# Performance work log

Hardware: AMD Instinct MI355X
Metric: run time of the kernel (lower is better)

Reference implementation:

```python
import jax, jax.numpy as jnp
import numpy as np
from jax import lax

# Config (matches init_kwargs)
E = 8         # num_routed_experts
K = 2         # topk
D = 2048      # d_model
H = 1408      # moe_hidden_dimension
NS = 2        # num_shared_experts
B, T = 2, 2048
EPS = 1e-20   # topk_norm_epsilon
HS = H * NS   # shared expert hidden dim


def setup_inputs() -> dict:
    key = jax.random.key(0)
    ks = jax.random.split(key, 8)
    s = 0.02
    return {
        "x": jax.random.normal(ks[0], (B, T, D), jnp.float32),
        "router_w": jax.random.normal(ks[1], (E, D), jnp.float32) * 0.006,
        # routed experts, stacked: gate/up: [E, D, H], down: [E, H, D]
        "wg": jax.random.normal(ks[2], (E, D, H), jnp.float32) * s,
        "wu": jax.random.normal(ks[3], (E, D, H), jnp.float32) * s,
        "wd": jax.random.normal(ks[4], (E, H, D), jnp.float32) * s,
        # shared expert (single big SwiGLU FFN)
        "sg": jax.random.normal(ks[5], (D, HS), jnp.float32) * s,
        "su": jax.random.normal(ks[6], (D, HS), jnp.float32) * s,
        "sd": jax.random.normal(ks[7], (HS, D), jnp.float32) * s,
    }


def _silu(v):
    return v * jax.nn.sigmoid(v)


def reference(x, router_w, wg, wu, wd, sg, su, sd):
    b, t, d = x.shape
    xf = x.reshape(b * t, d)                       # [N, D]
    n = xf.shape[0]

    # Router: softmax over experts, then top-k masking (DeepSeek style)
    gates = jax.nn.softmax(xf @ router_w.T, axis=-1)           # [N, E]
    topv, topi = lax.top_k(gates, K)                           # [N, K]
    masked = jnp.zeros_like(gates).at[jnp.arange(n)[:, None], topi].set(topv)
    # normalized_moe_gates=True
    masked = masked / (masked.sum(axis=-1, keepdims=True) + EPS)  # [N, E]

    # Per-expert SwiGLU FFN, weighted-accumulated over experts.
    # Mathematically identical to gather/grouped-GEMM/scatter-add combine:
    # tokens with zero gate for expert e contribute 0.
    def step(acc, p):
        wg_e, wu_e, wd_e, g_e = p                  # g_e: [N] gate weights
        y = (_silu(xf @ wg_e) * (xf @ wu_e)) @ wd_e  # [N, D]
        return acc + y * g_e[:, None], None

    routed, _ = lax.scan(step, jnp.zeros_like(xf), (wg, wu, wd, masked.T))

    # Shared experts (dense path applied to every token)
    shared = (_silu(xf @ sg) * (xf @ su)) @ sd      # [N, D]

    return (routed + shared).reshape(b, t, d)
```

## Files before the change

### kernel.cpp

```cpp
#include <hip/hip_runtime.h>
#include <hip/hip_bf16.h>
#include <cstdint>

#define NTOK 4096
#define DMODEL 2048
#define NEXP 8
#define HR 1408
#define HSHARED 2816
#define MAXT64 136
#define MAXT128 72

typedef __attribute__((ext_vector_type(8))) short bf16x8;
typedef __attribute__((ext_vector_type(4))) float f32x4;

__device__ inline unsigned short f2b(float f) {
    unsigned u = __float_as_uint(f);
    u += 0x7fffu + ((u >> 16) & 1u);
    return (unsigned short)(u >> 16);
}
__device__ inline unsigned pack2(float a, float b) {
    return (unsigned)f2b(a) | ((unsigned)f2b(b) << 16);
}

__device__ __forceinline__ void gll16(unsigned short* lds, const unsigned short* g) {
    __builtin_amdgcn_global_load_lds(
        (__attribute__((address_space(1))) void*)g,
        (__attribute__((address_space(3))) void*)lds, 16, 0, 0);
}

__global__ __launch_bounds__(256) void k_router(const float* __restrict__ x,
                                                const float* __restrict__ rw,
                                                int* __restrict__ topi,
                                                float* __restrict__ topw,
                                                int* __restrict__ counts) {
    int gw = (blockIdx.x * 256 + threadIdx.x) >> 6;
    int lane = threadIdx.x & 63;
    if (gw >= NTOK) return;
    const float* xr = x + (size_t)gw * DMODEL;
    float s[NEXP] = {0.f,0.f,0.f,0.f,0.f,0.f,0.f,0.f};
    for (int d = lane; d < DMODEL; d += 64) {
        float xv = xr[d];
#pragma unroll
        for (int e = 0; e < NEXP; e++) s[e] = fmaf(xv, rw[e * DMODEL + d], s[e]);
    }
#pragma unroll
    for (int e = 0; e < NEXP; e++)
        for (int o = 32; o > 0; o >>= 1) s[e] += __shfl_xor(s[e], o, 64);
    if (lane == 0) {
        int i1 = 0;
#pragma unroll
        for (int e = 1; e < NEXP; e++) if (s[e] > s[i1]) i1 = e;
        int i2 = (i1 == 0) ? 1 : 0;
#pragma unroll
        for (int e = 0; e < NEXP; e++) if (e != i1 && s[e] > s[i2]) i2 = e;
        float mx = s[0];
#pragma unroll
        for (int e = 1; e < NEXP; e++) mx = fmaxf(mx, s[e]);
        float den = 0.f, ex[NEXP];
#pragma unroll
        for (int e = 0; e < NEXP; e++) { ex[e] = __expf(s[e] - mx); den += ex[e]; }
        float v1 = ex[i1] / den, v2 = ex[i2] / den;
        float inv = 1.f / (v1 + v2 + 1e-20f);
        topi[2 * gw] = i1; topi[2 * gw + 1] = i2;
        topw[2 * gw] = v1 * inv; topw[2 * gw + 1] = v2 * inv;
        atomicAdd(&counts[i1], 1); atomicAdd(&counts[i2], 1);
    }
}

__global__ void k_scan(int* counts, int* offsets, int* cursors, int* ntiles,
                       int* tile_e, int* tile_r, int step) {
    if (threadIdx.x == 0 && blockIdx.x == 0) {
        int off = 0, nt = 0;
        for (int e = 0; e < NEXP; e++) {
            offsets[e] = off; cursors[e] = off;
            int c = counts[e];
            for (int r = 0; r < c; r += step) { tile_e[nt] = e; tile_r[nt] = r; nt++; }
            off += c;
        }
        ntiles[0] = nt;
    }
}

__global__ __launch_bounds__(256) void k_fill(const int* __restrict__ topi,
                                              const float* __restrict__ topw,
                                              int* cursors, int* at, float* aw) {
    int t = blockIdx.x * 256 + threadIdx.x;
    if (t >= NTOK) return;
#pragma unroll
    for (int k = 0; k < 2; k++) {
        int e = topi[2 * t + k];
        int pos = atomicAdd(&cursors[e], 1);
        at[pos] = t; aw[pos] = topw[2 * t + k];
    }
}

__global__ __launch_bounds__(256) void k_cvt_x(const float* __restrict__ src,
                                               unsigned short* __restrict__ dst) {
    size_t i = ((size_t)blockIdx.x * 256 + threadIdx.x) * 8;
    float4 a = *(const float4*)(src + i);
    float4 b = *(const float4*)(src + i + 4);
    uint4 v; v.x = pack2(a.x, a.y); v.y = pack2(a.z, a.w);
    v.z = pack2(b.x, b.y); v.w = pack2(b.z, b.w);
    *(uint4*)(dst + i) = v;
}

__global__ __launch_bounds__(256) void k_tcvt(const float* __restrict__ src,
                                              unsigned short* __restrict__ dst,
                                              int K, int N) {
    src += (size_t)blockIdx.z * K * N;
    dst += (size_t)blockIdx.z * K * N;
    int n0 = blockIdx.x * 64, k0 = blockIdx.y * 64;
    __shared__ unsigned short T[64][72];
    int t = threadIdx.x;
    int kr = t >> 4, nc = (t & 15) * 4;
#pragma unroll
    for (int i = 0; i < 4; i++) {
        int k = kr + i * 16;
        float4 v = *(const float4*)(src + (size_t)(k0 + k) * N + n0 + nc);
        T[k][nc] = f2b(v.x); T[k][nc + 1] = f2b(v.y);
        T[k][nc + 2] = f2b(v.z); T[k][nc + 3] = f2b(v.w);
    }
    __syncthreads();
    int nr = t >> 3, kc = (t & 7) * 8;
#pragma unroll
    for (int j = 0; j < 2; j++) {
        int n = nr + j * 32;
        unsigned short tmp[8];
#pragma unroll
        for (int u = 0; u < 8; u++) tmp[u] = T[kc + u][n];
        *(uint4*)(dst + (size_t)(n0 + n) * K + k0 + kc) = *(uint4*)tmp;
    }
}


template <bool GATHERED>
__global__ __launch_bounds__(256) void kf_gateup(
    const unsigned short* __restrict__ xb, const unsigned short* __restrict__ BgT,
    const unsigned short* __restrict__ BuT, int K, int Hld, int ebase,
    const int* __restrict__ tile_e, const int* __restrict__ tile_r,
    const int* __restrict__ offsets, const int* __restrict__ counts,
    const int* __restrict__ ntiles, const int* __restrict__ at,
    unsigned short* __restrict__ hout) {
    int m0, mcnt;
    const unsigned short* bgw = BgT;
    const unsigned short* buw = BuT;
    if (GATHERED) {
        if ((int)blockIdx.x >= ntiles[0]) return;
        int e = tile_e[blockIdx.x];
        if (e < ebase || e >= ebase + 4) return;
        int ro = tile_r[blockIdx.x];
        m0 = offsets[e] + ro;
        mcnt = counts[e] - ro; if (mcnt > 128) mcnt = 128;
        size_t wofs = (size_t)(e - ebase) * Hld * K;
        bgw += wofs; buw += wofs;
    } else { m0 = blockIdx.x * 128; mcnt = 128; }
    int n0 = blockIdx.y * 64;

    __shared__ __align__(16) unsigned short As[128 * 64];
    __shared__ __align__(16) unsigned short Bgs[64 * 64];
    __shared__ __align__(16) unsigned short Bus[64 * 64];

    int tid = threadIdx.x;
    int wv = tid >> 6, lane = tid & 63;
    int rbase = tid >> 3;
    int kc = (tid & 7) ^ ((tid >> 3) & 7);
    const unsigned short* arp[4];
#pragma unroll
    for (int j = 0; j < 4; j++) {
        int row = j * 32 + rbase;
        int cl = row < mcnt ? row : mcnt - 1;
        int grow = GATHERED ? at[m0 + cl] : (m0 + cl);
        arp[j] = xb + (size_t)grow * K + kc * 8;
    }
    const unsigned short* bgp[2];
    const unsigned short* bup[2];
#pragma unroll
    for (int j = 0; j < 2; j++) {
        int row = j * 32 + rbase;
        bgp[j] = bgw + (size_t)(n0 + row) * K + kc * 8;
        bup[j] = buw + (size_t)(n0 + row) * K + kc * 8;
    }
    unsigned short* a_l = As + (wv << 6) * 8;
    unsigned short* g_l = Bgs + (wv << 6) * 8;
    unsigned short* u_l = Bus + (wv << 6) * 8;

    int fr = lane & 15, quad = lane >> 4, sw = fr & 7;
    int wm = (wv & 1) << 6, wn = (wv >> 1) << 5;

    f32x4 accg[4][2] = {};
    f32x4 accu[4][2] = {};

    for (int k0 = 0; k0 < K; k0 += 64) {
        __syncthreads();
#pragma unroll
        for (int j = 0; j < 4; j++) gll16(a_l + j * 2048, arp[j] + k0);
#pragma unroll
        for (int j = 0; j < 2; j++) {
            gll16(g_l + j * 2048, bgp[j] + k0);
            gll16(u_l + j * 2048, bup[j] + k0);
        }
        __syncthreads();
#pragma unroll
        for (int s = 0; s < 2; s++) {
            int off = (((s << 2) + quad) ^ sw) << 3;
            bf16x8 a[4], g[2], u[2];
#pragma unroll
            for (int tm = 0; tm < 4; tm++)
                a[tm] = *(const bf16x8*)&As[(wm + tm * 16 + fr) * 64 + off];
#pragma unroll
            for (int tn = 0; tn < 2; tn++) {
                int rb = (wn + tn * 16 + fr) * 64 + off;
                g[tn] = *(const bf16x8*)&Bgs[rb];
                u[tn] = *(const bf16x8*)&Bus[rb];
            }
#pragma unroll
            for (int tm = 0; tm < 4; tm++)
#pragma unroll
                for (int tn = 0; tn < 2; tn++) {
                    accg[tm][tn] = __builtin_amdgcn_mfma_f32_16x16x32_bf16(a[tm], g[tn], accg[tm][tn], 0, 0, 0);
                    accu[tm][tn] = __builtin_amdgcn_mfma_f32_16x16x32_bf16(a[tm], u[tn], accu[tm][tn], 0, 0, 0);
                }
        }
    }
#pragma unroll
    for (int tm = 0; tm < 4; tm++)
#pragma unroll
        for (int r = 0; r < 4; r++) {
            int row = wm + tm * 16 + (quad << 2) + r;
            if (row < mcnt) {
#pragma unroll
                for (int tn = 0; tn < 2; tn++) {
                    float gv = accg[tm][tn][r], uv = accu[tm][tn][r];
                    float hv = (gv / (1.f + __expf(-gv))) * uv;
                    hout[(size_t)(m0 + row) * Hld + n0 + wn + tn * 16 + fr] = f2b(hv);
                }
            }
        }
}

template <bool GATHERED>
__global__ __launch_bounds__(256) void kf_down(
    const unsigned short* __restrict__ h, const unsigned short* __restrict__ BT,
    int K,
    const int* __restrict__ tile_e, const int* __restrict__ tile_r,
    const int* __restrict__ offsets, const int* __restrict__ counts,
    const int* __restrict__ ntiles, const int* __restrict__ at,
    const float* __restrict__ awt, float* __restrict__ out) {
    int m0, mcnt;
    const unsigned short* bw = BT;
    if (GATHERED) {
        if ((int)blockIdx.x >= ntiles[0]) return;
        int e = tile_e[blockIdx.x], ro = tile_r[blockIdx.x];
        m0 = offsets[e] + ro;
        mcnt = counts[e] - ro; if (mcnt > 128) mcnt = 128;
        bw += (size_t)e * DMODEL * K;
    } else { m0 = blockIdx.x * 128; mcnt = 128; }
    int n0 = blockIdx.y * 128;

    __shared__ __align__(16) unsigned short As[128 * 64];
    __shared__ __align__(16) unsigned short Bs[128 * 64];

    int tid = threadIdx.x;
    int wv = tid >> 6, lane = tid & 63;
    int rbase = tid >> 3;
    int kc = (tid & 7) ^ ((tid >> 3) & 7);
    const unsigned short* arp[4];
    const unsigned short* brp[4];
#pragma unroll
    for (int j = 0; j < 4; j++) {
        int row = j * 32 + rbase;
        int cl = row < mcnt ? row : mcnt - 1;
        arp[j] = h + (size_t)(m0 + cl) * K + kc * 8;
        brp[j] = bw + (size_t)(n0 + row) * K + kc * 8;
    }
    unsigned short* a_l = As + (wv << 6) * 8;
    unsigned short* b_l = Bs + (wv << 6) * 8;

    int fr = lane & 15, quad = lane >> 4, sw = fr & 7;
    int wm = (wv & 1) << 6, wn = (wv >> 1) << 6;

    f32x4 acc[4][4] = {};

    for (int k0 = 0; k0 < K; k0 += 64) {
        __syncthreads();
#pragma unroll
        for (int j = 0; j < 4; j++) {
            gll16(a_l + j * 2048, arp[j] + k0);
            gll16(b_l + j * 2048, brp[j] + k0);
        }
        __syncthreads();
#pragma unroll
        for (int s = 0; s < 2; s++) {
            int off = (((s << 2) + quad) ^ sw) << 3;
            bf16x8 a[4], b[4];
#pragma unroll
            for (int tm = 0; tm < 4; tm++)
                a[tm] = *(const bf16x8*)&As[(wm + tm * 16 + fr) * 64 + off];
#pragma unroll
            for (int tn = 0; tn < 4; tn++)
                b[tn] = *(const bf16x8*)&Bs[(wn + tn * 16 + fr) * 64 + off];
#pragma unroll
            for (int tm = 0; tm < 4; tm++)
#pragma unroll
                for (int tn = 0; tn < 4; tn++)
                    acc[tm][tn] = __builtin_amdgcn_mfma_f32_16x16x32_bf16(a[tm], b[tn], acc[tm][tn], 0, 0, 0);
        }
    }
#pragma unroll
    for (int tm = 0; tm < 4; tm++)
#pragma unroll
        for (int r = 0; r < 4; r++) {
            int row = wm + tm * 16 + (quad << 2) + r;
            if (row < mcnt) {
                if (GATHERED) {
                    int tok = at[m0 + row];
                    float w = awt[m0 + row];
#pragma unroll
                    for (int tn = 0; tn < 4; tn++)
                        atomicAdd(&out[(size_t)tok * DMODEL + n0 + wn + tn * 16 + fr],
                                  w * acc[tm][tn][r]);
                } else {
#pragma unroll
                    for (int tn = 0; tn < 4; tn++)
                        out[(size_t)(m0 + row) * DMODEL + n0 + wn + tn * 16 + fr] =
                            acc[tm][tn][r];
                }
            }
        }
}

template <bool GATHERED>
__global__ __launch_bounds__(256) void k_gateup(
    const float* __restrict__ x, const float* __restrict__ Wg,
    const float* __restrict__ Wu, int Hld,
    const int* __restrict__ tile_e, const int* __restrict__ tile_r,
    const int* __restrict__ offsets, const int* __restrict__ counts,
    const int* __restrict__ ntiles, const int* __restrict__ at,
    unsigned short* __restrict__ hout) {
    int m0, mcnt;
    const float* wgp = Wg;
    const float* wup = Wu;
    if (GATHERED) {
        if ((int)blockIdx.x >= ntiles[0]) return;
        int e = tile_e[blockIdx.x], ro = tile_r[blockIdx.x];
        m0 = offsets[e] + ro;
        mcnt = counts[e] - ro; if (mcnt > 64) mcnt = 64;
        size_t wofs = (size_t)e * DMODEL * Hld;
        wgp += wofs; wup += wofs;
    } else { m0 = blockIdx.x * 64; mcnt = 64; }
    int n0 = blockIdx.y * 64;
    __shared__ unsigned short As[64][48];
    __shared__ unsigned short Bgs[64][48];
    __shared__ unsigned short Bus[64][48];
    int tid = threadIdx.x;
    int ai = tid >> 2, ak = (tid & 3) << 3;
    int arowi = m0 + (ai < mcnt ? ai : (mcnt - 1));
    const float* arow = x + (size_t)(GATHERED ? at[arowi] : arowi) * DMODEL;
    int bn = tid >> 2, bk = (tid & 3) << 1;
    const float* bcolg = wgp + (size_t)n0 + bn;
    const float* bcolu = wup + (size_t)n0 + bn;
    int lane = tid & 63, wv = tid >> 6;
    int wm = (wv & 1) << 5, wn = (wv >> 1) << 5;
    int fr = lane & 15, fk = (lane >> 4) << 3;
    f32x4 accg[2][2] = {};
    f32x4 accu[2][2] = {};
    for (int k0 = 0; k0 < DMODEL; k0 += 32) {
        __syncthreads();
        float4 a0 = *(const float4*)(arow + k0 + ak);
        float4 a1 = *(const float4*)(arow + k0 + ak + 4);
        uint4 av; av.x = pack2(a0.x, a0.y); av.y = pack2(a0.z, a0.w);
        av.z = pack2(a1.x, a1.y); av.w = pack2(a1.z, a1.w);
        *(uint4*)&As[ai][ak] = av;
#pragma unroll
        for (int j = 0; j < 4; j++) {
            int kk = bk + (j << 3);
            size_t o0 = (size_t)(k0 + kk) * Hld;
            *(unsigned*)&Bgs[bn][kk] = pack2(bcolg[o0], bcolg[o0 + Hld]);
            *(unsigned*)&Bus[bn][kk] = pack2(bcolu[o0], bcolu[o0 + Hld]);
        }
        __syncthreads();
        bf16x8 af[2], bg[2], bu[2];
#pragma unroll
        for (int t = 0; t < 2; t++) {
            af[t] = *(bf16x8*)&As[wm + t * 16 + fr][fk];
            bg[t] = *(bf16x8*)&Bgs[wn + t * 16 + fr][fk];
            bu[t] = *(bf16x8*)&Bus[wn + t * 16 + fr][fk];
        }
#pragma unroll
        for (int tm = 0; tm < 2; tm++)
#pragma unroll
            for (int tn = 0; tn < 2; tn++) {
                accg[tm][tn] = __builtin_amdgcn_mfma_f32_16x16x32_bf16(af[tm], bg[tn], accg[tm][tn], 0, 0, 0);
                accu[tm][tn] = __builtin_amdgcn_mfma_f32_16x16x32_bf16(af[tm], bu[tn], accu[tm][tn], 0, 0, 0);
            }
    }
    int quad = (lane >> 4) << 2;
#pragma unroll
    for (int tm = 0; tm < 2; tm++)
#pragma unroll
        for (int r = 0; r < 4; r++) {
            int row = wm + tm * 16 + quad + r;
            if (row < mcnt) {
#pragma unroll
                for (int tn = 0; tn < 2; tn++) {
                    float g = accg[tm][tn][r], u = accu[tm][tn][r];
                    float hv = (g / (1.f + __expf(-g))) * u;
                    hout[(size_t)(m0 + row) * Hld + n0 + wn + tn * 16 + fr] = f2b(hv);
                }
            }
        }
}

template <bool GATHERED>
__global__ __launch_bounds__(256) void k_down(
    const unsigned short* __restrict__ h, const float* __restrict__ Wd, int Hld,
    const int* __restrict__ tile_e, const int* __restrict__ tile_r,
    const int* __restrict__ offsets, const int* __restrict__ counts,
    const int* __restrict__ ntiles, const int* __restrict__ at,
    const float* __restrict__ aw, float* __restrict__ out) {
    int m0, mcnt;
    const float* wdp = Wd;
    if (GATHERED) {
        if ((int)blockIdx.x >= ntiles[0]) return;
        int e = tile_e[blockIdx.x], ro = tile_r[blockIdx.x];
        m0 = offsets[e] + ro;
        mcnt = counts[e] - ro; if (mcnt > 64) mcnt = 64;
        wdp += (size_t)e * Hld * DMODEL;
    } else { m0 = blockIdx.x * 64; mcnt = 64; }
    int n0 = blockIdx.y * 64;
    __shared__ unsigned short As[64][48];
    __shared__ unsigned short Bs[64][48];
    int tid = threadIdx.x;
    int ai = tid >> 2, ak = (tid & 3) << 3;
    const unsigned short* arow = h + (size_t)(m0 + (ai < mcnt ? ai : (mcnt - 1))) * Hld;
    int bn = tid >> 2, bk = (tid & 3) << 1;
    const float* bcol = wdp + (size_t)n0 + bn;
    int lane = tid & 63, wv = tid >> 6;
    int wm = (wv & 1) << 5, wn = (wv >> 1) << 5;
    int fr = lane & 15, fk = (lane >> 4) << 3;
    f32x4 acc[2][2] = {};
    for (int k0 = 0; k0 < Hld; k0 += 32) {
        __syncthreads();
        *(uint4*)&As[ai][ak] = *(const uint4*)(arow + k0 + ak);
#pragma unroll
        for (int j = 0; j < 4; j++) {
            int kk = bk + (j << 3);
            size_t o0 = (size_t)(k0 + kk) * DMODEL;
            *(unsigned*)&Bs[bn][kk] = pack2(bcol[o0], bcol[o0 + DMODEL]);
        }
        __syncthreads();
        bf16x8 af[2], bf[2];
#pragma unroll
        for (int t = 0; t < 2; t++) {
            af[t] = *(bf16x8*)&As[wm + t * 16 + fr][fk];
            bf[t] = *(bf16x8*)&Bs[wn + t * 16 + fr][fk];
        }
#pragma unroll
        for (int tm = 0; tm < 2; tm++)
#pragma unroll
            for (int tn = 0; tn < 2; tn++)
                acc[tm][tn] = __builtin_amdgcn_mfma_f32_16x16x32_bf16(af[tm], bf[tn], acc[tm][tn], 0, 0, 0);
    }
    int quad = (lane >> 4) << 2;
#pragma unroll
    for (int tm = 0; tm < 2; tm++)
#pragma unroll
        for (int r = 0; r < 4; r++) {
            int row = wm + tm * 16 + quad + r;
            if (row < mcnt) {
                int mrow = m0 + row;
                int tok = GATHERED ? at[mrow] : mrow;
                float w = GATHERED ? aw[mrow] : 1.f;
#pragma unroll
                for (int tn = 0; tn < 2; tn++)
                    atomicAdd(&out[(size_t)tok * DMODEL + n0 + wn + tn * 16 + fr],
                              w * acc[tm][tn][r]);
            }
        }
}

extern "C" void kernel_launch(void* const* d_in, const int* in_sizes, int n_in,
                              void* d_out, int out_size, void* d_ws, size_t ws_size,
                              hipStream_t stream) {
    (void)in_sizes; (void)n_in;
    const float* x  = (const float*)d_in[0];
    const float* rw = (const float*)d_in[1];
    const float* wg = (const float*)d_in[2];
    const float* wu = (const float*)d_in[3];
    const float* wd = (const float*)d_in[4];
    const float* sg = (const float*)d_in[5];
    const float* su = (const float*)d_in[6];
    const float* sd = (const float*)d_in[7];
    float* out = (float*)d_out;

    int* counts  = (int*)d_ws;
    int* offsets = counts + 8;
    int* cursors = counts + 16;
    int* ntiles  = counts + 24;
    int* tile_e  = counts + 32;
    int* tile_r  = tile_e + 144;
    int* topi    = tile_r + 144;
    float* topw  = (float*)(topi + 8192);
    int* at      = (int*)(topw + 8192);
    float* aw    = (float*)(at + 8192);

    const size_t META = 262144;
    const size_t XB   = (size_t)NTOK * DMODEL * 2;
    const size_t POOL_NEED = 69206016;
    const size_t FAST_NEED = META + XB + POOL_NEED;
    bool fast = ws_size >= FAST_NEED;

    hipMemsetAsync(counts, 0, 32, stream);
    k_router<<<dim3(NTOK / 4), 256, 0, stream>>>(x, rw, topi, topw, counts);
    k_scan<<<1, 64, 0, stream>>>(counts, offsets, cursors, ntiles, tile_e, tile_r,
                                 fast ? 128 : 64);
    k_fill<<<dim3(NTOK / 256), 256, 0, stream>>>(topi, topw, cursors, at, aw);

    if (fast) {
        char* base = (char*)d_ws;
        unsigned short* xb = (unsigned short*)(base + META);
        char* pool = base + META + XB;
        unsigned short* sgT = (unsigned short*)pool;
        unsigned short* suT = (unsigned short*)(pool + 11534336);
        unsigned short* h_s = (unsigned short*)(pool + 23068672);
        unsigned short* sdT = (unsigned short*)(pool + 46137344);
        unsigned short* wgT = (unsigned short*)pool;
        unsigned short* wuT = (unsigned short*)(pool + 23068672);
        unsigned short* h_r = (unsigned short*)(pool + 46137344);
        unsigned short* wdT = (unsigned short*)pool;

        k_cvt_x<<<dim3(4096), 256, 0, stream>>>(x, xb);

        k_tcvt<<<dim3(HSHARED / 64, DMODEL / 64, 1), 256, 0, stream>>>(sg, sgT, DMODEL, HSHARED);
        k_tcvt<<<dim3(HSHARED / 64, DMODEL / 64, 1), 256, 0, stream>>>(su, suT, DMODEL, HSHARED);
        kf_gateup<false><<<dim3(NTOK / 128, HSHARED / 64), 256, 0, stream>>>(
            xb, sgT, suT, DMODEL, HSHARED, 0,
            nullptr, nullptr, nullptr, nullptr, nullptr, nullptr, h_s);
        k_tcvt<<<dim3(DMODEL / 64, HSHARED / 64, 1), 256, 0, stream>>>(sd, sdT, HSHARED, DMODEL);
        kf_down<false><<<dim3(NTOK / 128, DMODEL / 128), 256, 0, stream>>>(
            h_s, sdT, HSHARED,
            nullptr, nullptr, nullptr, nullptr, nullptr, nullptr, nullptr, out);

        k_tcvt<<<dim3(HR / 64, DMODEL / 64, 4), 256, 0, stream>>>(wg, wgT, DMODEL, HR);
        k_tcvt<<<dim3(HR / 64, DMODEL / 64, 4), 256, 0, stream>>>(wu, wuT, DMODEL, HR);
        kf_gateup<true><<<dim3(MAXT128, HR / 64), 256, 0, stream>>>(
            xb, wgT, wuT, DMODEL, HR, 0,
            tile_e, tile_r, offsets, counts, ntiles, at, h_r);
        k_tcvt<<<dim3(HR / 64, DMODEL / 64, 4), 256, 0, stream>>>(
            wg + (size_t)4 * DMODEL * HR, wgT, DMODEL, HR);
        k_tcvt<<<dim3(HR / 64, DMODEL / 64, 4), 256, 0, stream>>>(
            wu + (size_t)4 * DMODEL * HR, wuT, DMODEL, HR);
        kf_gateup<true><<<dim3(MAXT128, HR / 64), 256, 0, stream>>>(
            xb, wgT, wuT, DMODEL, HR, 4,
            tile_e, tile_r, offsets, counts, ntiles, at, h_r);
        k_tcvt<<<dim3(DMODEL / 64, HR / 64, 8), 256, 0, stream>>>(wd, wdT, HR, DMODEL);
        kf_down<true><<<dim3(MAXT128, DMODEL / 128), 256, 0, stream>>>(
            h_r, wdT, HR,
            tile_e, tile_r, offsets, counts, ntiles, at, aw, out);
    } else {
        unsigned short* h_r =
            (unsigned short*)(((uintptr_t)(aw + 8192) + 255) & ~(uintptr_t)255);
        unsigned short* h_s = h_r + (size_t)8192 * HR;
        hipMemsetAsync(out, 0, (size_t)out_size * sizeof(float), stream);
        k_gateup<true><<<dim3(MAXT64, HR / 64), 256, 0, stream>>>(
            x, wg, wu, HR, tile_e, tile_r, offsets, counts, ntiles, at, h_r);
        k_gateup<false><<<dim3(NTOK / 64, HSHARED / 64), 256, 0, stream>>>(
            x, sg, su, HSHARED, nullptr, nullptr, nullptr, nullptr, nullptr, nullptr, h_s);
        k_down<true><<<dim3(MAXT64, DMODEL / 64), 256, 0, stream>>>(
            h_r, wd, HR, tile_e, tile_r, offsets, counts, ntiles, at, aw, out);
        k_down<false><<<dim3(NTOK / 64, DMODEL / 64), 256, 0, stream>>>(
            h_s, sd, HSHARED, nullptr, nullptr, nullptr, nullptr, nullptr, nullptr, nullptr, out);
    }
}
```

Measured before the change: 957.5 us.

## Split routed down-proj by top-k slot to replace atomics with plain adds

The router now counts first-choice and second-choice assignments separately, and the scan builds two tile lists so each token appears at most once per list. The routed down projection runs as two launches, one per top-k slot, and each does a plain read-modify-write instead of atomicAdd on the output, which is meant to cut atomic traffic. The router also stages router weights in LDS and handles two tokens per wave with vector loads. The cost is an extra kernel launch and possibly more partial tiles across the two lists.

```diff
diff --git a/kernel.cpp b/kernel.cpp
--- a/kernel.cpp
+++ b/kernel.cpp
@@ -9,6 +9,8 @@
 #define HSHARED 2816
 #define MAXT64 136
 #define MAXT128 72
+#define NDT 48
+#define DGRID 40
 
 typedef __attribute__((ext_vector_type(8))) short bf16x8;
 typedef __attribute__((ext_vector_type(4))) float f32x4;
@@ -32,66 +34,93 @@
                                                 const float* __restrict__ rw,
                                                 int* __restrict__ topi,
                                                 float* __restrict__ topw,
-                                                int* __restrict__ counts) {
-    int gw = (blockIdx.x * 256 + threadIdx.x) >> 6;
-    int lane = threadIdx.x & 63;
-    if (gw >= NTOK) return;
-    const float* xr = x + (size_t)gw * DMODEL;
-    float s[NEXP] = {0.f,0.f,0.f,0.f,0.f,0.f,0.f,0.f};
-    for (int d = lane; d < DMODEL; d += 64) {
-        float xv = xr[d];
-#pragma unroll
-        for (int e = 0; e < NEXP; e++) s[e] = fmaf(xv, rw[e * DMODEL + d], s[e]);
-    }
-#pragma unroll
-    for (int e = 0; e < NEXP; e++)
-        for (int o = 32; o > 0; o >>= 1) s[e] += __shfl_xor(s[e], o, 64);
-    if (lane == 0) {
-        int i1 = 0;
-#pragma unroll
-        for (int e = 1; e < NEXP; e++) if (s[e] > s[i1]) i1 = e;
-        int i2 = (i1 == 0) ? 1 : 0;
-#pragma unroll
-        for (int e = 0; e < NEXP; e++) if (e != i1 && s[e] > s[i2]) i2 = e;
-        float mx = s[0];
-#pragma unroll
-        for (int e = 1; e < NEXP; e++) mx = fmaxf(mx, s[e]);
-        float den = 0.f, ex[NEXP];
-#pragma unroll
-        for (int e = 0; e < NEXP; e++) { ex[e] = __expf(s[e] - mx); den += ex[e]; }
-        float v1 = ex[i1] / den, v2 = ex[i2] / den;
-        float inv = 1.f / (v1 + v2 + 1e-20f);
-        topi[2 * gw] = i1; topi[2 * gw + 1] = i2;
-        topw[2 * gw] = v1 * inv; topw[2 * gw + 1] = v2 * inv;
-        atomicAdd(&counts[i1], 1); atomicAdd(&counts[i2], 1);
-    }
-}
-
-__global__ void k_scan(int* counts, int* offsets, int* cursors, int* ntiles,
-                       int* tile_e, int* tile_r, int step) {
+                                                int* __restrict__ c0,
+                                                int* __restrict__ c1) {
+    __shared__ float lrw[NEXP * DMODEL];
+    int tid = threadIdx.x;
+#pragma unroll
+    for (int i = 0; i < (NEXP * DMODEL / 4) / 256; i++) {
+        int idx = (i * 256 + tid) * 4;
+        *(float4*)&lrw[idx] = *(const float4*)&rw[idx];
+    }
+    __syncthreads();
+    int wv = tid >> 6, lane = tid & 63;
+#pragma unroll
+    for (int tt = 0; tt < 2; tt++) {
+        int t = blockIdx.x * 8 + wv * 2 + tt;
+        const float* xr = x + (size_t)t * DMODEL;
+        float s[NEXP] = {0.f,0.f,0.f,0.f,0.f,0.f,0.f,0.f};
+#pragma unroll 2
+        for (int i = 0; i < 8; i++) {
+            int d = (lane << 2) + (i << 8);
+            float4 xv = *(const float4*)(xr + d);
+#pragma unroll
+            for (int e = 0; e < NEXP; e++) {
+                float4 w4 = *(const float4*)&lrw[e * DMODEL + d];
+                s[e] += xv.x * w4.x + xv.y * w4.y + xv.z * w4.z + xv.w * w4.w;
+            }
+        }
+#pragma unroll
+        for (int e = 0; e < NEXP; e++)
+#pragma unroll
+            for (int o = 32; o > 0; o >>= 1) s[e] += __shfl_xor(s[e], o, 64);
+        if (lane == 0) {
+            int i1 = 0;
+#pragma unroll
+            for (int e = 1; e < NEXP; e++) if (s[e] > s[i1]) i1 = e;
+            int i2 = (i1 == 0) ? 1 : 0;
+#pragma unroll
+            for (int e = 0; e < NEXP; e++) if (e != i1 && s[e] > s[i2]) i2 = e;
+            float mx = s[0];
+#pragma unroll
+            for (int e = 1; e < NEXP; e++) mx = fmaxf(mx, s[e]);
+            float den = 0.f, ex[NEXP];
+#pragma unroll
+            for (int e = 0; e < NEXP; e++) { ex[e] = __expf(s[e] - mx); den += ex[e]; }
+            float v1 = ex[i1] / den, v2 = ex[i2] / den;
+            float inv = 1.f / (v1 + v2 + 1e-20f);
+            topi[2 * t] = i1; topi[2 * t + 1] = i2;
+            topw[2 * t] = v1 * inv; topw[2 * t + 1] = v2 * inv;
+            atomicAdd(&c0[i1], 1); atomicAdd(&c1[i2], 1);
+        }
+    }
+}
+
+__global__ void k_scan(const int* __restrict__ c0, const int* __restrict__ c1,
+                       int* ccomb, int* offsets, int* cur0, int* cur1, int* ntl,
+                       int* gt_e, int* gt_r,
+                       int* dt_e, int* dt_m0, int* dt_cnt, int gstep) {
     if (threadIdx.x == 0 && blockIdx.x == 0) {
-        int off = 0, nt = 0;
+        int off = 0, ngt = 0, nd0 = 0, nd1 = 0;
         for (int e = 0; e < NEXP; e++) {
-            offsets[e] = off; cursors[e] = off;
-            int c = counts[e];
-            for (int r = 0; r < c; r += step) { tile_e[nt] = e; tile_r[nt] = r; nt++; }
+            int a = c0[e], b = c1[e], c = a + b;
+            ccomb[e] = c; offsets[e] = off; cur0[e] = off; cur1[e] = off + a;
+            for (int r = 0; r < c; r += gstep) { gt_e[ngt] = e; gt_r[ngt] = r; ngt++; }
+            for (int r = 0; r < a; r += 128) {
+                dt_e[nd0] = e; dt_m0[nd0] = off + r;
+                dt_cnt[nd0] = (a - r < 128) ? (a - r) : 128; nd0++;
+            }
+            for (int r = 0; r < b; r += 128) {
+                dt_e[NDT + nd1] = e; dt_m0[NDT + nd1] = off + a + r;
+                dt_cnt[NDT + nd1] = (b - r < 128) ? (b - r) : 128; nd1++;
+            }
             off += c;
         }
-        ntiles[0] = nt;
+        ntl[0] = ngt; ntl[1] = nd0; ntl[2] = nd1;
     }
 }
 
 __global__ __launch_bounds__(256) void k_fill(const int* __restrict__ topi,
                                               const float* __restrict__ topw,
-                                              int* cursors, int* at, float* aw) {
+                                              int* cur0, int* cur1,
+                                              int* at, float* aw) {
     int t = blockIdx.x * 256 + threadIdx.x;
     if (t >= NTOK) return;
-#pragma unroll
-    for (int k = 0; k < 2; k++) {
-        int e = topi[2 * t + k];
-        int pos = atomicAdd(&cursors[e], 1);
-        at[pos] = t; aw[pos] = topw[2 * t + k];
-    }
+    int e1 = topi[2 * t], e2 = topi[2 * t + 1];
+    int p0 = atomicAdd(&cur0[e1], 1);
+    at[p0] = t; aw[p0] = topw[2 * t];
+    int p1 = atomicAdd(&cur1[e2], 1);
+    at[p1] = t; aw[p1] = topw[2 * t + 1];
 }
 
 __global__ __launch_bounds__(256) void k_cvt_x(const float* __restrict__ src,
@@ -242,17 +271,17 @@
 __global__ __launch_bounds__(256) void kf_down(
     const unsigned short* __restrict__ h, const unsigned short* __restrict__ BT,
     int K,
-    const int* __restrict__ tile_e, const int* __restrict__ tile_r,
-    const int* __restrict__ offsets, const int* __restrict__ counts,
-    const int* __restrict__ ntiles, const int* __restrict__ at,
-    const float* __restrict__ awt, float* __restrict__ out) {
+    const int* __restrict__ dt_e, const int* __restrict__ dt_m0,
+    const int* __restrict__ dt_cnt, const int* __restrict__ nd,
+    const int* __restrict__ at, const float* __restrict__ awt,
+    float* __restrict__ out) {
     int m0, mcnt;
     const unsigned short* bw = BT;
     if (GATHERED) {
-        if ((int)blockIdx.x >= ntiles[0]) return;
-        int e = tile_e[blockIdx.x], ro = tile_r[blockIdx.x];
-        m0 = offsets[e] + ro;
-        mcnt = counts[e] - ro; if (mcnt > 128) mcnt = 128;
+        if ((int)blockIdx.x >= nd[0]) return;
+        int e = dt_e[blockIdx.x];
+        m0 = dt_m0[blockIdx.x];
+        mcnt = dt_cnt[blockIdx.x];
         bw += (size_t)e * DMODEL * K;
     } else { m0 = blockIdx.x * 128; mcnt = 128; }
     int n0 = blockIdx.y * 128;
@@ -316,9 +345,10 @@
                     int tok = at[m0 + row];
                     float w = awt[m0 + row];
 #pragma unroll
-                    for (int tn = 0; tn < 4; tn++)
-                        atomicAdd(&out[(size_t)tok * DMODEL + n0 + wn + tn * 16 + fr],
-                                  w * acc[tm][tn][r]);
+                    for (int tn = 0; tn < 4; tn++) {
+                        float* op = &out[(size_t)tok * DMODEL + n0 + wn + tn * 16 + fr];
+                        *op += w * acc[tm][tn][r];
+                    }
                 } else {
 #pragma unroll
                     for (int tn = 0; tn < 4; tn++)
@@ -493,16 +523,23 @@
     const float* sd = (const float*)d_in[7];
     float* out = (float*)d_out;
 
-    int* counts  = (int*)d_ws;
-    int* offsets = counts + 8;
-    int* cursors = counts + 16;
-    int* ntiles  = counts + 24;
-    int* tile_e  = counts + 32;
-    int* tile_r  = tile_e + 144;
-    int* topi    = tile_r + 144;
-    float* topw  = (float*)(topi + 8192);
-    int* at      = (int*)(topw + 8192);
-    float* aw    = (float*)(at + 8192);
+    int* meta    = (int*)d_ws;
+    int* c0      = meta;
+    int* c1      = meta + 8;
+    int* ccomb   = meta + 16;
+    int* offsets = meta + 24;
+    int* cur0    = meta + 32;
+    int* cur1    = meta + 40;
+    int* ntl     = meta + 48;
+    int* gt_e    = meta + 64;
+    int* gt_r    = meta + 208;
+    int* dt_e    = meta + 352;
+    int* dt_m0   = meta + 448;
+    int* dt_cnt  = meta + 544;
+    int* topi    = meta + 640;
+    float* topw  = (float*)(meta + 8832);
+    int* at      = meta + 17024;
+    float* aw    = (float*)(meta + 25216);
 
     const size_t META = 262144;
     const size_t XB   = (size_t)NTOK * DMODEL * 2;
@@ -510,11 +547,11 @@
     const size_t FAST_NEED = META + XB + POOL_NEED;
     bool fast = ws_size >= FAST_NEED;
 
-    hipMemsetAsync(counts, 0, 32, stream);
-    k_router<<<dim3(NTOK / 4), 256, 0, stream>>>(x, rw, topi, topw, counts);
-    k_scan<<<1, 64, 0, stream>>>(counts, offsets, cursors, ntiles, tile_e, tile_r,
-                                 fast ? 128 : 64);
-    k_fill<<<dim3(NTOK / 256), 256, 0, stream>>>(topi, topw, cursors, at, aw);
+    hipMemsetAsync(c0, 0, 64, stream);
+    k_router<<<dim3(NTOK / 8), 256, 0, stream>>>(x, rw, topi, topw, c0, c1);
+    k_scan<<<1, 64, 0, stream>>>(c0, c1, ccomb, offsets, cur0, cur1, ntl,
+                                 gt_e, gt_r, dt_e, dt_m0, dt_cnt, fast ? 128 : 64);
+    k_fill<<<dim3(NTOK / 256), 256, 0, stream>>>(topi, topw, cur0, cur1, at, aw);
 
     if (fast) {
         char* base = (char*)d_ws;
@@ -539,36 +576,38 @@
         k_tcvt<<<dim3(DMODEL / 64, HSHARED / 64, 1), 256, 0, stream>>>(sd, sdT, HSHARED, DMODEL);
         kf_down<false><<<dim3(NTOK / 128, DMODEL / 128), 256, 0, stream>>>(
             h_s, sdT, HSHARED,
-            nullptr, nullptr, nullptr, nullptr, nullptr, nullptr, nullptr, out);
+            nullptr, nullptr, nullptr, nullptr, nullptr, nullptr, out);
 
         k_tcvt<<<dim3(HR / 64, DMODEL / 64, 4), 256, 0, stream>>>(wg, wgT, DMODEL, HR);
         k_tcvt<<<dim3(HR / 64, DMODEL / 64, 4), 256, 0, stream>>>(wu, wuT, DMODEL, HR);
         kf_gateup<true><<<dim3(MAXT128, HR / 64), 256, 0, stream>>>(
             xb, wgT, wuT, DMODEL, HR, 0,
-            tile_e, tile_r, offsets, counts, ntiles, at, h_r);
+            gt_e, gt_r, offsets, ccomb, ntl, at, h_r);
         k_tcvt<<<dim3(HR / 64, DMODEL / 64, 4), 256, 0, stream>>>(
             wg + (size_t)4 * DMODEL * HR, wgT, DMODEL, HR);
         k_tcvt<<<dim3(HR / 64, DMODEL / 64, 4), 256, 0, stream>>>(
             wu + (size_t)4 * DMODEL * HR, wuT, DMODEL, HR);
         kf_gateup<true><<<dim3(MAXT128, HR / 64), 256, 0, stream>>>(
             xb, wgT, wuT, DMODEL, HR, 4,
-            tile_e, tile_r, offsets, counts, ntiles, at, h_r);
+            gt_e, gt_r, offsets, ccomb, ntl, at, h_r);
         k_tcvt<<<dim3(DMODEL / 64, HR / 64, 8), 256, 0, stream>>>(wd, wdT, HR, DMODEL);
-        kf_down<true><<<dim3(MAXT128, DMODEL / 128), 256, 0, stream>>>(
-            h_r, wdT, HR,
-            tile_e, tile_r, offsets, counts, ntiles, at, aw, out);
+        kf_down<true><<<dim3(DGRID, DMODEL / 128), 256, 0, stream>>>(
+            h_r, wdT, HR, dt_e, dt_m0, dt_cnt, ntl + 1, at, aw, out);
+        kf_down<true><<<dim3(DGRID, DMODEL / 128), 256, 0, stream>>>(
+            h_r, wdT, HR, dt_e + NDT, dt_m0 + NDT, dt_cnt + NDT, ntl + 2, at, aw, out);
     } else {
         unsigned short* h_r =
             (unsigned short*)(((uintptr_t)(aw + 8192) + 255) & ~(uintptr_t)255);
         unsigned short* h_s = h_r + (size_t)8192 * HR;
         hipMemsetAsync(out, 0, (size_t)out_size * sizeof(float), stream);
         k_gateup<true><<<dim3(MAXT64, HR / 64), 256, 0, stream>>>(
-            x, wg, wu, HR, tile_e, tile_r, offsets, counts, ntiles, at, h_r);
+            x, wg, wu, HR, gt_e, gt_r, offsets, ccomb, ntl, at, h_r);
         k_gateup<false><<<dim3(NTOK / 64, HSHARED / 64), 256, 0, stream>>>(
             x, sg, su, HSHARED, nullptr, nullptr, nullptr, nullptr, nullptr, nullptr, h_s);
         k_down<true><<<dim3(MAXT64, DMODEL / 64), 256, 0, stream>>>(
-            h_r, wd, HR, tile_e, tile_r, offsets, counts, ntiles, at, aw, out);
+            h_r, wd, HR, gt_e, gt_r, offsets, ccomb, ntl, at, aw, out);
         k_down<false><<<dim3(NTOK / 64, DMODEL / 64), 256, 0, stream>>>(
-            h_s, sd, HSHARED, nullptr, nullptr, nullptr, nullptr, nullptr, nullptr, nullptr, out);
-    }
-}
+            h_s, sd, HSHARED,
+            nullptr, nullptr, nullptr, nullptr, nullptr, nullptr, nullptr, out);
+    }
+}
```

After: 941.5 us. About the same (-1.7%).
